# Performance work log

Hardware: AMD Instinct MI355X
Metric: run time of the kernel (lower is better)

Reference implementation:

```python
import jax, jax.numpy as jnp
import numpy as np

# --- sizes / simulation constants (match init_kwargs) ---
IN_F, OUT_F, BIAS = 512, 512, 1
BATCH = 128
RES, SIM_TIME, TAU_SYN = 1e-4, 2e-2, 5e-3
STEPS = int(np.ceil(SIM_TIME / RES))                 # 200
DECAY_SYN = float(np.exp(-RES / TAU_SYN))
DECAY_MEM = float(np.exp(-RES / TAU_SYN))            # original code uses tau_syn for both


def setup_inputs() -> dict:
    key = jax.random.key(0)
    k1, k2, k3, k4 = jax.random.split(key, 4)
    # input spikes inside the first half of the sim window
    input_times = jax.random.uniform(k1, (BATCH, IN_F), jnp.float32) * (0.5 * SIM_TIME)
    # weights_init = (0.05, 0.1) normal
    weights = 0.05 + 0.1 * jax.random.normal(k2, (IN_F + BIAS, OUT_F), jnp.float32)
    # delays_init = (0.001, 0.0005) normal, kept non-negative
    delays = jnp.abs(0.001 + 0.0005 * jax.random.normal(k3, (IN_F + BIAS, OUT_F), jnp.float32))
    # thresholds_init = (1.0, 0.05) normal
    thresholds = 1.0 + 0.05 * jax.random.normal(k4, (OUT_F,), jnp.float32)
    return {"input_times": input_times, "weights": weights,
            "delays": delays, "thresholds": thresholds}


def _snn_forward(input_times, weights, delays, thresholds):
    B = input_times.shape[0]
    dt = input_times.dtype
    # bias inputs spike at t = 0
    times = jnp.concatenate([input_times, jnp.zeros((B, BIAS), dt)], axis=1)   # [B, I+bias]
    # per-synapse delayed arrival times -> time-step indices
    arrival = times[:, :, None] + delays[None]                                  # [B, I+bias, O]
    step_idx = jnp.clip(jnp.round(arrival / RES).astype(jnp.int32), 0, STEPS - 1)
    b_idx = jnp.arange(B)[:, None, None]
    o_idx = jnp.arange(OUT_F)[None, None, :]
    w = jnp.broadcast_to(weights[None], arrival.shape)
    # charge[b, t, o] = sum_i w[i,o] * 1[arrival step of synapse (i,o) == t]
    charge = jnp.zeros((B, STEPS, OUT_F), dt).at[b_idx, step_idx, o_idx].add(w)
    charge = jnp.moveaxis(charge, 1, 0)                                         # [steps, B, O]

    thr = thresholds[None]                                                      # [1, O]

    def body(carry, inp):
        syn, mem, spike_t, spiked = carry
        t, c = inp
        syn_n = syn * DECAY_SYN + c
        mem_n = mem * DECAY_MEM + (1.0 - DECAY_MEM) * syn_n
        crossing = jnp.logical_and(~spiked, mem_n >= thr)
        denom = mem_n - mem
        safe = jnp.where(jnp.abs(denom) > 1e-12, denom, 1e-12)
        frac = jnp.clip((thr - mem) / safe, 0.0, 1.0)     # linear interp inside the step
        t_cross = (t + frac) * RES
        spike_t = jnp.where(crossing, t_cross, spike_t)
        spiked = jnp.logical_or(spiked, crossing)
        return (syn_n, mem_n, spike_t, spiked), None

    init = (jnp.zeros((B, OUT_F), dt),
            jnp.zeros((B, OUT_F), dt),
            jnp.full((B, OUT_F), SIM_TIME, dt),           # "no spike" -> sim_time
            jnp.zeros((B, OUT_F), bool))
    ts = jnp.arange(STEPS, dtype=dt)
    (syn, mem, spike_t, spiked), _ = jax.lax.scan(body, init, (ts, charge))
    return spike_t                                        # [B, O] first-spike times


def reference(input_times, weights, delays, thresholds):
    return _snn_forward(input_times, weights, delays, thresholds)
```

## Files before the change

### kernel.cpp

```cpp
#include <hip/hip_runtime.h>


#define IN_F    512
#define OUT_F   512
#define BATCH   128
#define STEPS   200
#define RES_F   1e-4f
#define CSTRIDE 65
#define DECAY_F 0.98019867330675525f
#define ONEMD_F 0.019801326693244747f
#define SIM_T_F 2e-2f
#define FPSCALE 8388608.0f
#define INVSCALE 1.1920928955078125e-07f

__device__ __forceinline__ int bin_of(float arr) {
    float q = (float)((double)arr * 10000.0);
    int s = __float2int_rn(q);
    s = s < 0 ? 0 : (s > STEPS - 1 ? STEPS - 1 : s);
    return s;
}

__global__ __launch_bounds__(256) void prep_wi(
    const float* __restrict__ weights, int* __restrict__ wI)
{
    int idx = blockIdx.x * 256 + threadIdx.x;
    if (idx < (IN_F + 1) * OUT_F / 4) {
        float4 v = ((const float4*)weights)[idx];
        int4 r;
        r.x = __float2int_rn(v.x * FPSCALE);
        r.y = __float2int_rn(v.y * FPSCALE);
        r.z = __float2int_rn(v.z * FPSCALE);
        r.w = __float2int_rn(v.w * FPSCALE);
        ((int4*)wI)[idx] = r;
    }
}

__global__ __launch_bounds__(512, 6) void snn_fwd(
    const float* __restrict__ input_times,
    const int*   __restrict__ wI,
    const float* __restrict__ delays,
    const float* __restrict__ thresholds,
    float* __restrict__ out)
{
#pragma clang fp contract(off)
    __shared__ __align__(16) int chargeI[STEPS * CSTRIDE];
    __shared__ float times_s[IN_F];

    const int tid  = threadIdx.x;
    const int wv   = tid >> 6;
    const int lane = tid & 63;
    const int b     = blockIdx.x >> 3;
    const int otile = blockIdx.x & 7;
    const int ob    = otile << 6;

    {
        int4 z = make_int4(0, 0, 0, 0);
        int4* c4 = (int4*)chargeI;
        #pragma unroll
        for (int k = tid; k < (STEPS * CSTRIDE) / 4; k += 512) c4[k] = z;
    }
    times_s[tid] = input_times[b * IN_F + tid];
    __syncthreads();

    const int sub = lane >> 4;
    const int cg  = (lane & 15) << 2;
    const int4*   __restrict__ Wp = (const int4*)wI;
    const float4* __restrict__ Dp = (const float4*)delays;
    const int r0   = wv << 6;
    const int i0   = (r0 + sub) * (OUT_F / 4) + ((ob + cg) >> 2);
    const int gstr = 4 * (OUT_F / 4);

    if (wv == 7) {
        float dl = delays[IN_F * OUT_F + ob + lane];
        int   wt = wI[IN_F * OUT_F + ob + lane];
        atomicAdd(&chargeI[bin_of(dl) * CSTRIDE + lane], wt);
    }

    int4   wA = Wp[i0],            wB = Wp[i0 + gstr];
    float4 dA = Dp[i0],            dB = Dp[i0 + gstr];
    float  tA = times_s[r0 + sub];
    float  tB = times_s[r0 + 4 + sub];

    #pragma unroll
    for (int g = 0; g < 16; g += 2) {
        int4   wC = {}, wD = {};
        float4 dC = {}, dD = {};
        float  tC = 0.f, tD = 0.f;
        if (g + 2 < 16) {
            wC = Wp[i0 + (g + 2) * gstr]; dC = Dp[i0 + (g + 2) * gstr];
            tC = times_s[r0 + ((g + 2) << 2) + sub];
        }
        if (g + 3 < 16) {
            wD = Wp[i0 + (g + 3) * gstr]; dD = Dp[i0 + (g + 3) * gstr];
            tD = times_s[r0 + ((g + 3) << 2) + sub];
        }
        {
            const float* dv = (const float*)&dA;
            const int*   wi = (const int*)&wA;
            #pragma unroll
            for (int k = 0; k < 4; ++k) {
                int s = bin_of(tA + dv[k]);
                atomicAdd(&chargeI[s * CSTRIDE + cg + k], wi[k]);
            }
        }
        {
            const float* dv = (const float*)&dB;
            const int*   wi = (const int*)&wB;
            #pragma unroll
            for (int k = 0; k < 4; ++k) {
                int s = bin_of(tB + dv[k]);
                atomicAdd(&chargeI[s * CSTRIDE + cg + k], wi[k]);
            }
        }
        wA = wC; dA = dC; tA = tC;
        wB = wD; dB = dD; tB = tD;
    }
    __syncthreads();

    if (wv == 0) {
        const float thr = thresholds[ob + lane];
        float syn = 0.f, mem = 0.f, spike_t = SIM_T_F;
        bool spiked = false;
        for (int t0 = 0; t0 < STEPS; t0 += 4) {
            float c[4];
            #pragma unroll
            for (int j = 0; j < 4; ++j)
                c[j] = (float)chargeI[(t0 + j) * CSTRIDE + lane] * INVSCALE;
            #pragma unroll
            for (int j = 0; j < 4; ++j) {
                float syn_n = syn * DECAY_F + c[j];
                float mem_n = mem * DECAY_F + ONEMD_F * syn_n;
                if (!spiked && mem_n >= thr) {
                    float denom = mem_n - mem;
                    float safe  = fabsf(denom) > 1e-12f ? denom : 1e-12f;
                    float frac  = (thr - mem) / safe;
                    frac = frac < 0.f ? 0.f : (frac > 1.f ? 1.f : frac);
                    spike_t = ((float)(t0 + j) + frac) * RES_F;
                    spiked  = true;
                }
                syn = syn_n; mem = mem_n;
            }
            if (__all(spiked)) break;
        }
        out[b * OUT_F + ob + lane] = spike_t;
    }
}

extern "C" void kernel_launch(void* const* d_in, const int* in_sizes, int n_in,
                              void* d_out, int out_size, void* d_ws, size_t ws_size,
                              hipStream_t stream) {
    const float* input_times = (const float*)d_in[0];
    const float* weights     = (const float*)d_in[1];
    const float* delays      = (const float*)d_in[2];
    const float* thresholds  = (const float*)d_in[3];
    float* out = (float*)d_out;
    int*   wI  = (int*)d_ws;

    int nvec4 = (IN_F + 1) * OUT_F / 4;
    prep_wi<<<(nvec4 + 255) / 256, 256, 0, stream>>>(weights, wI);

    dim3 grid(BATCH * (OUT_F / 64));
    snn_fwd<<<grid, 512, 0, stream>>>(input_times, wI, delays, thresholds, out);
}
```

Baseline: 79.04 us.

## Split time bins into two passes to shrink LDS and skip late bins

The charge histogram in shared memory now holds only the first 144 time steps, which cuts LDS per block and allows the launch bound to go from 6 to 8 blocks per CU. The membrane scan runs over those steps first. Only if some neuron in the tile has not yet spiked does the block re-zero the buffer, re-bin the remaining late steps and finish the scan. The cost is a second pass of global weight and delay loads plus binning whenever any neuron is still silent, and the late pass is only skipped when every lane has already spiked.

```diff
diff --git a/kernel.cpp b/kernel.cpp
--- a/kernel.cpp
+++ b/kernel.cpp
@@ -5,6 +5,8 @@
 #define OUT_F   512
 #define BATCH   128
 #define STEPS   200
+#define SPLIT   144
+#define ROWS_B  (STEPS - SPLIT)
 #define RES_F   1e-4f
 #define CSTRIDE 65
 #define DECAY_F 0.98019867330675525f
@@ -35,47 +37,12 @@
     }
 }
 
-__global__ __launch_bounds__(512, 6) void snn_fwd(
-    const float* __restrict__ input_times,
-    const int*   __restrict__ wI,
-    const float* __restrict__ delays,
-    const float* __restrict__ thresholds,
-    float* __restrict__ out)
+template<bool PASSB>
+__device__ __forceinline__ void bin_pass(
+    const int4* __restrict__ Wp, const float4* __restrict__ Dp,
+    const float* __restrict__ times_s, int* __restrict__ chargeI,
+    int i0, int gstr, int r0, int sub, int cg)
 {
-#pragma clang fp contract(off)
-    __shared__ __align__(16) int chargeI[STEPS * CSTRIDE];
-    __shared__ float times_s[IN_F];
-
-    const int tid  = threadIdx.x;
-    const int wv   = tid >> 6;
-    const int lane = tid & 63;
-    const int b     = blockIdx.x >> 3;
-    const int otile = blockIdx.x & 7;
-    const int ob    = otile << 6;
-
-    {
-        int4 z = make_int4(0, 0, 0, 0);
-        int4* c4 = (int4*)chargeI;
-        #pragma unroll
-        for (int k = tid; k < (STEPS * CSTRIDE) / 4; k += 512) c4[k] = z;
-    }
-    times_s[tid] = input_times[b * IN_F + tid];
-    __syncthreads();
-
-    const int sub = lane >> 4;
-    const int cg  = (lane & 15) << 2;
-    const int4*   __restrict__ Wp = (const int4*)wI;
-    const float4* __restrict__ Dp = (const float4*)delays;
-    const int r0   = wv << 6;
-    const int i0   = (r0 + sub) * (OUT_F / 4) + ((ob + cg) >> 2);
-    const int gstr = 4 * (OUT_F / 4);
-
-    if (wv == 7) {
-        float dl = delays[IN_F * OUT_F + ob + lane];
-        int   wt = wI[IN_F * OUT_F + ob + lane];
-        atomicAdd(&chargeI[bin_of(dl) * CSTRIDE + lane], wt);
-    }
-
     int4   wA = Wp[i0],            wB = Wp[i0 + gstr];
     float4 dA = Dp[i0],            dB = Dp[i0 + gstr];
     float  tA = times_s[r0 + sub];
@@ -100,7 +67,10 @@
             #pragma unroll
             for (int k = 0; k < 4; ++k) {
                 int s = bin_of(tA + dv[k]);
-                atomicAdd(&chargeI[s * CSTRIDE + cg + k], wi[k]);
+                if (!PASSB) { if (s < SPLIT)
+                    atomicAdd(&chargeI[s * CSTRIDE + cg + k], wi[k]); }
+                else        { if (s >= SPLIT)
+                    atomicAdd(&chargeI[(s - SPLIT) * CSTRIDE + cg + k], wi[k]); }
             }
         }
         {
@@ -109,19 +79,67 @@
             #pragma unroll
             for (int k = 0; k < 4; ++k) {
                 int s = bin_of(tB + dv[k]);
-                atomicAdd(&chargeI[s * CSTRIDE + cg + k], wi[k]);
+                if (!PASSB) { if (s < SPLIT)
+                    atomicAdd(&chargeI[s * CSTRIDE + cg + k], wi[k]); }
+                else        { if (s >= SPLIT)
+                    atomicAdd(&chargeI[(s - SPLIT) * CSTRIDE + cg + k], wi[k]); }
             }
         }
         wA = wC; dA = dC; tA = tC;
         wB = wD; dB = dD; tB = tD;
     }
+}
+
+__global__ __launch_bounds__(512, 8) void snn_fwd(
+    const float* __restrict__ input_times,
+    const int*   __restrict__ wI,
+    const float* __restrict__ delays,
+    const float* __restrict__ thresholds,
+    float* __restrict__ out)
+{
+#pragma clang fp contract(off)
+    __shared__ __align__(16) int chargeI[SPLIT * CSTRIDE];
+    __shared__ float times_s[IN_F];
+    __shared__ int alldone_s;
+
+    const int tid  = threadIdx.x;
+    const int wv   = tid >> 6;
+    const int lane = tid & 63;
+    const int b     = blockIdx.x >> 3;
+    const int otile = blockIdx.x & 7;
+    const int ob    = otile << 6;
+
+    {
+        int4 z = make_int4(0, 0, 0, 0);
+        int4* c4 = (int4*)chargeI;
+        #pragma unroll
+        for (int k = tid; k < (SPLIT * CSTRIDE) / 4; k += 512) c4[k] = z;
+    }
+    times_s[tid] = input_times[b * IN_F + tid];
     __syncthreads();
 
+    const int sub = lane >> 4;
+    const int cg  = (lane & 15) << 2;
+    const int4*   __restrict__ Wp = (const int4*)wI;
+    const float4* __restrict__ Dp = (const float4*)delays;
+    const int r0   = wv << 6;
+    const int i0   = (r0 + sub) * (OUT_F / 4) + ((ob + cg) >> 2);
+    const int gstr = 4 * (OUT_F / 4);
+
+    if (wv == 7) {
+        float dl = delays[IN_F * OUT_F + ob + lane];
+        int   wt = wI[IN_F * OUT_F + ob + lane];
+        int s = bin_of(dl);
+        if (s < SPLIT) atomicAdd(&chargeI[s * CSTRIDE + lane], wt);
+    }
+    bin_pass<false>(Wp, Dp, times_s, chargeI, i0, gstr, r0, sub, cg);
+    __syncthreads();
+
+    const float thr = (wv == 0) ? thresholds[ob + lane] : 0.f;
+    float syn = 0.f, mem = 0.f, spike_t = SIM_T_F;
+    bool spiked = false;
     if (wv == 0) {
-        const float thr = thresholds[ob + lane];
-        float syn = 0.f, mem = 0.f, spike_t = SIM_T_F;
-        bool spiked = false;
-        for (int t0 = 0; t0 < STEPS; t0 += 4) {
+        for (int t0 = 0; t0 < SPLIT; t0 += 4) {
             float c[4];
             #pragma unroll
             for (int j = 0; j < 4; ++j)
@@ -142,8 +160,53 @@
             }
             if (__all(spiked)) break;
         }
-        out[b * OUT_F + ob + lane] = spike_t;
-    }
+        int ad = __all(spiked) ? 1 : 0;
+        if (lane == 0) alldone_s = ad;
+    }
+    __syncthreads();
+
+    if (!alldone_s) {
+        {
+            int4 z = make_int4(0, 0, 0, 0);
+            int4* c4 = (int4*)chargeI;
+            for (int k = tid; k < (ROWS_B * CSTRIDE) / 4; k += 512) c4[k] = z;
+        }
+        __syncthreads();
+        if (wv == 7) {
+            float dl = delays[IN_F * OUT_F + ob + lane];
+            int   wt = wI[IN_F * OUT_F + ob + lane];
+            int s = bin_of(dl);
+            if (s >= SPLIT)
+                atomicAdd(&chargeI[(s - SPLIT) * CSTRIDE + lane], wt);
+        }
+        bin_pass<true>(Wp, Dp, times_s, chargeI, i0, gstr, r0, sub, cg);
+        __syncthreads();
+        if (wv == 0) {
+            for (int t0 = SPLIT; t0 < STEPS; t0 += 4) {
+                float c[4];
+                #pragma unroll
+                for (int j = 0; j < 4; ++j)
+                    c[j] = (float)chargeI[(t0 - SPLIT + j) * CSTRIDE + lane]
+                           * INVSCALE;
+                #pragma unroll
+                for (int j = 0; j < 4; ++j) {
+                    float syn_n = syn * DECAY_F + c[j];
+                    float mem_n = mem * DECAY_F + ONEMD_F * syn_n;
+                    if (!spiked && mem_n >= thr) {
+                        float denom = mem_n - mem;
+                        float safe  = fabsf(denom) > 1e-12f ? denom : 1e-12f;
+                        float frac  = (thr - mem) / safe;
+                        frac = frac < 0.f ? 0.f : (frac > 1.f ? 1.f : frac);
+                        spike_t = ((float)(t0 + j) + frac) * RES_F;
+                        spiked  = true;
+                    }
+                    syn = syn_n; mem = mem_n;
+                }
+                if (__all(spiked)) break;
+            }
+        }
+    }
+    if (wv == 0) out[b * OUT_F + ob + lane] = spike_t;
 }
 
 extern "C" void kernel_launch(void* const* d_in, const int* in_sizes, int n_in,
```

New measurement: 192.3 us. +143.3%, slower.
